# Kernel tuning notes

Hardware: AMD Instinct MI355X
Metric: run time of the kernel (lower is better)

Reference implementation:

```python
import jax, jax.numpy as jnp
import numpy as np

EPS = 1e-5

def layer_norm(x, w, b):
    mu = jnp.mean(x, axis=-1, keepdims=True)
    var = jnp.mean(jnp.square(x - mu), axis=-1, keepdims=True)
    return (x - mu) * jax.lax.rsqrt(var + EPS) * w + b

def setup_inputs() -> dict:
    key = jax.random.key(0)
    ks = jax.random.split(key, 16)
    B, N, c_z, c_h = 1, 512, 128, 128
    s_z = 1.0 / np.sqrt(c_z)
    s_h = 1.0 / np.sqrt(c_h)
    return {
        "z": jax.random.normal(ks[0], (B, N, N, c_z), jnp.float32),
        "mask": jnp.ones((B, N, N), jnp.float32),
        "norm_in_w": jnp.ones((c_z,), jnp.float32),
        "norm_in_b": jnp.zeros((c_z,), jnp.float32),
        "a_p_w": jax.random.normal(ks[1], (c_h, c_z), jnp.float32) * s_z,
        "a_p_b": jnp.zeros((c_h,), jnp.float32),
        "a_g_w": jax.random.normal(ks[2], (c_h, c_z), jnp.float32) * s_z,
        "a_g_b": jnp.ones((c_h,), jnp.float32),
        "b_p_w": jax.random.normal(ks[3], (c_h, c_z), jnp.float32) * s_z,
        "b_p_b": jnp.zeros((c_h,), jnp.float32),
        "b_g_w": jax.random.normal(ks[4], (c_h, c_z), jnp.float32) * s_z,
        "b_g_b": jnp.ones((c_h,), jnp.float32),
        "g_w": jax.random.normal(ks[5], (c_z, c_z), jnp.float32) * s_z,
        "g_b": jnp.ones((c_z,), jnp.float32),
        "z_w": jax.random.normal(ks[6], (c_z, c_h), jnp.float32) * s_h,
        "z_b": jnp.zeros((c_z,), jnp.float32),
        "norm_out_w": jnp.ones((c_h,), jnp.float32),
        "norm_out_b": jnp.zeros((c_h,), jnp.float32),
    }

OUTGOING = True

def reference(z, mask, norm_in_w, norm_in_b, a_p_w, a_p_b, a_g_w, a_g_b,
              b_p_w, b_p_b, b_g_w, b_g_b, g_w, g_b, z_w, z_b,
              norm_out_w, norm_out_b):
    # z: [B, N, N, c_z]; mask: [B, N, N]
    m = mask[..., None]  # [B, N, N, 1]
    zn = layer_norm(z, norm_in_w, norm_in_b)
    # gated projections (nn.Linear layout: W is [out, in])
    a = m * jax.nn.sigmoid(zn @ a_g_w.T + a_g_b) * (zn @ a_p_w.T + a_p_b)
    b = m * jax.nn.sigmoid(zn @ b_g_w.T + b_g_b) * (zn @ b_p_w.T + b_p_b)
    if OUTGOING:
        # x[i,j,c] = sum_k a[i,k,c] * b[j,k,c]
        x = jnp.einsum('bikc,bjkc->bijc', a, b)
    else:
        x = jnp.einsum('bkic,bkjc->bijc', a, b)
    x = layer_norm(x, norm_out_w, norm_out_b)
    x = x @ z_w.T + z_b
    g = jax.nn.sigmoid(zn @ g_w.T + g_b)
    return x * g
```

## Files before the change

### kernel.cpp

```cpp
#include <hip/hip_runtime.h>
#include <stddef.h>

#define NN 512
#define CC 128
#define NPOS (NN*NN)
#define CPITCH (NPOS + 512)

typedef unsigned short u16;
typedef unsigned int   u32;
typedef u16  u16x4  __attribute__((ext_vector_type(4)));
typedef u16  u16x8  __attribute__((ext_vector_type(8)));
typedef __bf16 bf16x8 __attribute__((ext_vector_type(8)));
typedef float f32x4  __attribute__((ext_vector_type(4)));

__device__ __forceinline__ float b2f(u16 u) {
    union { u32 i; float f; } w; w.i = ((u32)u) << 16; return w.f;
}
__device__ __forceinline__ u16 f2b(float f) {
    return __builtin_bit_cast(u16, (__bf16)f);
}
__device__ __forceinline__ float sigm(float x) { return 1.0f / (1.0f + __expf(-x)); }

__device__ __forceinline__ void gld16(const u16* g, u16* l) {
    __builtin_amdgcn_global_load_lds(
        (const __attribute__((address_space(1))) u32*)g,
        (__attribute__((address_space(3))) u32*)l, 16, 0, 0);
}

struct W6 { const float* p[6]; };

__global__ __launch_bounds__(256) void k0_pack(W6 w, u16* __restrict__ dst)
{
    const int i = blockIdx.x * 256 + threadIdx.x;
    const int mt = i >> 14, r = i & 16383;
    const int cb = r >> 11, ks = (r >> 9) & 3, lane = (r >> 3) & 63, j = r & 7;
    const int row = cb * 16 + (lane & 15);
    const int col = ks * 32 + (lane >> 4) * 8 + j;
    dst[i] = f2b(w.p[mt][row * 128 + col]);
}

__global__ __launch_bounds__(512) void k1_ln_proj(
    const float* __restrict__ z,  const float* __restrict__ mask,
    const float* __restrict__ wi, const float* __restrict__ bi,
    const u16* __restrict__ wpk,
    const float* __restrict__ agb, const float* __restrict__ apb,
    const float* __restrict__ bgb, const float* __restrict__ bpb,
    u16* __restrict__ a_cm, u16* __restrict__ b_cm,
    u16* __restrict__ zn_pm)
{
    __shared__ u16   zn[128][136];
    __shared__ float mk_lds[128];
    const int tid = threadIdx.x;
    const size_t p0 = (size_t)blockIdx.x * 128;

    if (tid < 128) mk_lds[tid] = mask[p0 + tid];

    {
        const int g  = tid >> 5;
        const int c4 = (tid & 31) * 4;
        const f32x4 wi4 = *(const f32x4*)(wi + c4);
        const f32x4 bi4 = *(const f32x4*)(bi + c4);
        f32x4 v[8];
        #pragma unroll
        for (int h = 0; h < 8; ++h)
            v[h] = *(const f32x4*)(z + (p0 + h * 16 + g) * CC + c4);
        #pragma unroll
        for (int h = 0; h < 8; ++h) {
            float s  = (v[h][0] + v[h][1]) + (v[h][2] + v[h][3]);
            float s2 = (v[h][0]*v[h][0] + v[h][1]*v[h][1])
                     + (v[h][2]*v[h][2] + v[h][3]*v[h][3]);
            #pragma unroll
            for (int ms = 1; ms <= 16; ms <<= 1) {
                s  += __shfl_xor(s,  ms);
                s2 += __shfl_xor(s2, ms);
            }
            const float mu   = s * (1.0f / CC);
            const float rstd = rsqrtf(s2 * (1.0f / CC) - mu * mu + 1e-5f);
            u16x4 o4;
            #pragma unroll
            for (int e = 0; e < 4; ++e) {
                const float nw = rstd * wi4[e];
                o4[e] = f2b(v[h][e] * nw + __builtin_fmaf(-mu, nw, bi4[e]));
            }
            const int row = h * 16 + g;
            *(u16x4*)&zn[row][c4] = o4;
            if (zn_pm)
                *(u16x4*)(zn_pm + (p0 + row) * CC + c4) = o4;
        }
    }

    const int wave = tid >> 6, lane = tid & 63;
    const int m = lane & 15, q = lane >> 4;
    const int cb = wave;
    const int o  = cb * 16 + m;

    bf16x8 wreg[4][4];
    float  bias4[4];
    {
        const float* Bv[4] = { agb, apb, bgb, bpb };
        #pragma unroll
        for (int mt = 0; mt < 4; ++mt) {
            bias4[mt] = Bv[mt][o];
            const u16* wp = wpk + ((size_t)((mt * 8 + cb) * 4)) * 512
                                + (size_t)lane * 8;
            #pragma unroll
            for (int ks = 0; ks < 4; ++ks)
                wreg[mt][ks] = *(const bf16x8*)(wp + ks * 512);
        }
    }
    __syncthreads();

    #pragma unroll 2
    for (int t = 0; t < 8; ++t) {
        bf16x8 af[4];
        #pragma unroll
        for (int ks = 0; ks < 4; ++ks)
            af[ks] = *(const bf16x8*)&zn[t * 16 + m][ks * 32 + q * 8];
        const f32x4 mk4 = *(const f32x4*)&mk_lds[t * 16 + q * 4];

        f32x4 res[4];
        #pragma unroll
        for (int mt = 0; mt < 4; ++mt) {
            const float bv = bias4[mt];
            res[mt] = f32x4{ bv, bv, bv, bv };
        }
        #pragma unroll
        for (int ks = 0; ks < 4; ++ks)
            #pragma unroll
            for (int mt = 0; mt < 4; ++mt)
                res[mt] = __builtin_amdgcn_mfma_f32_16x16x32_bf16(
                            af[ks], wreg[mt][ks], res[mt], 0, 0, 0);

        u16x4 av, bv;
        #pragma unroll
        for (int r = 0; r < 4; ++r) {
            const float mk = mk4[r];
            av[r] = f2b(mk * sigm(res[0][r]) * res[1][r]);
            bv[r] = f2b(mk * sigm(res[2][r]) * res[3][r]);
        }
        const size_t off = (size_t)o * CPITCH + p0 + t * 16 + q * 4;
        *(u16x4*)(a_cm + off) = av;
        *(u16x4*)(b_cm + off) = bv;
    }
}

__global__ __launch_bounds__(256) void k2_gemm(
    const u16* __restrict__ A, const u16* __restrict__ B, u16* __restrict__ X)
{
    __shared__ u16 As[2][128][32];
    __shared__ u16 Bs[2][128][32];
    const int tid = threadIdx.x;
    const int bx  = blockIdx.x;
    const int xcd  = bx & 7;
    const int slot = bx >> 3;
    const int c    = (slot >> 4) * 8 + xcd;
    const int tile = slot & 15;
    const int i0   = (tile >> 2) * 128;
    const int j0   = (tile & 3) * 128;
    const size_t cbase = (size_t)c * CPITCH;
    const u16* Ac = A + cbase;
    const u16* Bc = B + cbase;

    const int wave = tid >> 6, lane = tid & 63;
    const int wm = wave >> 1, wn = wave & 1;
    const int m = lane & 15, q = lane >> 4;

    f32x4 acc[4][4];
    const f32x4 zero = { 0.f, 0.f, 0.f, 0.f };
    #pragma unroll
    for (int mt = 0; mt < 4; ++mt)
        #pragma unroll
        for (int nt = 0; nt < 4; ++nt) acc[mt][nt] = zero;

    auto stage = [&](int kt, int buf) {
        #pragma unroll
        for (int ps = 0; ps < 2; ++ps) {
            const int id = ps * 256 + tid;
            const int rw = id >> 2;
            const int g  = (id & 3) ^ ((rw >> 1) & 3);
            const size_t goff = (size_t)(kt * 32 + g * 8);
            gld16(Ac + (size_t)(i0 + rw) * NN + goff, &As[buf][0][0] + id * 8);
            gld16(Bc + (size_t)(j0 + rw) * NN + goff, &Bs[buf][0][0] + id * 8);
        }
    };
    auto compute = [&](int buf) {
        bf16x8 af[4], bf[4];
        #pragma unroll
        for (int mt = 0; mt < 4; ++mt) {
            const int row = wm * 64 + mt * 16 + m;
            const int slt = q ^ ((row >> 1) & 3);
            af[mt] = *(const bf16x8*)&As[buf][row][slt * 8];
        }
        #pragma unroll
        for (int nt = 0; nt < 4; ++nt) {
            const int row = wn * 64 + nt * 16 + m;
            const int slt = q ^ ((row >> 1) & 3);
            bf[nt] = *(const bf16x8*)&Bs[buf][row][slt * 8];
        }
        #pragma unroll
        for (int mt = 0; mt < 4; ++mt)
            #pragma unroll
            for (int nt = 0; nt < 4; ++nt)
                acc[mt][nt] = __builtin_amdgcn_mfma_f32_16x16x32_bf16(
                                af[mt], bf[nt], acc[mt][nt], 0, 0, 0);
    };

    stage(0, 0);
    int cur = 0;
    for (int kt = 0; kt < 15; ++kt) {
        stage(kt + 1, cur ^ 1);
        asm volatile("s_waitcnt vmcnt(4)" ::: "memory");
        __builtin_amdgcn_s_barrier();
        __builtin_amdgcn_sched_barrier(0);
        compute(cur);
        __builtin_amdgcn_sched_barrier(0);
        __builtin_amdgcn_s_barrier();
        cur ^= 1;
    }
    asm volatile("s_waitcnt vmcnt(0)" ::: "memory");
    __builtin_amdgcn_s_barrier();
    __builtin_amdgcn_sched_barrier(0);
    compute(cur);

    #pragma unroll
    for (int mt = 0; mt < 4; ++mt) {
        #pragma unroll
        for (int r = 0; r < 4; ++r) {
            const int i = i0 + wm * 64 + mt * 16 + q * 4 + r;
            #pragma unroll
            for (int nt = 0; nt < 4; ++nt) {
                const int j = j0 + wn * 64 + nt * 16 + m;
                X[cbase + (size_t)i * NN + j] = f2b(acc[mt][nt][r]);
            }
        }
    }
}

__global__ __launch_bounds__(256) void k3_out_zn(
    float* __restrict__ out, const u16* __restrict__ x_cm,
    const u16* __restrict__ zn_pm,
    const float* __restrict__ wo, const float* __restrict__ bo,
    const u16* __restrict__ wpk,
    const float* __restrict__ gbv, const float* __restrict__ zbv)
{
    __shared__ u16 A[128][136];
    __shared__ u16 Bt[128][136];
    const int tid = threadIdx.x;
    const size_t p0 = (size_t)blockIdx.x * 128;
    const int wave = tid >> 6, lane = tid & 63;
    const int m = lane & 15, q = lane >> 4;
    const int pl = tid >> 1, ht = tid & 1;

    {
        const int c = tid >> 1, seg = tid & 1;
        #pragma unroll
        for (int e = 0; e < 8; ++e) {
            u16x8 vv = *(const u16x8*)(x_cm + (size_t)c * CPITCH + p0 + seg * 64 + e * 8);
            *(u16x8*)&Bt[c][seg * 64 + e * 8] = vv;
        }
    }
    bf16x8 afz[2][4];
    #pragma unroll
    for (int t = 0; t < 2; ++t)
        #pragma unroll
        for (int ks = 0; ks < 4; ++ks)
            afz[t][ks] = *(const bf16x8*)(zn_pm
                           + (p0 + wave * 32 + t * 16 + m) * CC + ks * 32 + q * 8);
    __syncthreads();

    {
        float v[64];
        #pragma unroll
        for (int e = 0; e < 64; ++e) v[e] = b2f(Bt[ht * 64 + e][pl]);
        float s = 0.f, s2 = 0.f;
        #pragma unroll
        for (int e = 0; e < 64; ++e) { s += v[e]; s2 += v[e] * v[e]; }
        s  += __shfl_xor(s, 1);
        s2 += __shfl_xor(s2, 1);
        const float mu   = s * (1.0f / CC);
        const float rstd = rsqrtf(s2 * (1.0f / CC) - mu * mu + 1e-5f);
        #pragma unroll
        for (int h = 0; h < 8; ++h) {
            u16x8 o8;
            #pragma unroll
            for (int e = 0; e < 8; ++e) {
                const int c = ht * 64 + h * 8 + e;
                o8[e] = f2b((v[h * 8 + e] - mu) * rstd * wo[c] + bo[c]);
            }
            *(u16x8*)&A[pl][ht * 64 + h * 8] = o8;
        }
    }
    __syncthreads();

    bf16x8 afx[2][4];
    #pragma unroll
    for (int t = 0; t < 2; ++t)
        #pragma unroll
        for (int ks = 0; ks < 4; ++ks)
            afx[t][ks] = *(const bf16x8*)&A[wave * 32 + t * 16 + m][ks * 32 + q * 8];

    for (int cb = 0; cb < 8; ++cb) {
        const int o = cb * 16 + m;
        const float gb0 = gbv[o], zb0 = zbv[o];
        f32x4 accg[2], accx[2];
        #pragma unroll
        for (int t = 0; t < 2; ++t) {
            accg[t] = f32x4{ gb0, gb0, gb0, gb0 };
            accx[t] = f32x4{ zb0, zb0, zb0, zb0 };
        }
        const u16* wpg = wpk + ((size_t)((4 * 8 + cb) * 4)) * 512 + (size_t)lane * 8;
        const u16* wpz = wpk + ((size_t)((5 * 8 + cb) * 4)) * 512 + (size_t)lane * 8;
        bf16x8 wg[4], wz[4];
        #pragma unroll
        for (int ks = 0; ks < 4; ++ks) {
            wg[ks] = *(const bf16x8*)(wpg + ks * 512);
            wz[ks] = *(const bf16x8*)(wpz + ks * 512);
        }
        #pragma unroll
        for (int ks = 0; ks < 4; ++ks)
            #pragma unroll
            for (int t = 0; t < 2; ++t) {
                accg[t] = __builtin_amdgcn_mfma_f32_16x16x32_bf16(
                            afz[t][ks], wg[ks], accg[t], 0, 0, 0);
                accx[t] = __builtin_amdgcn_mfma_f32_16x16x32_bf16(
                            afx[t][ks], wz[ks], accx[t], 0, 0, 0);
            }
        #pragma unroll
        for (int t = 0; t < 2; ++t)
            #pragma unroll
            for (int r = 0; r < 4; ++r) {
                const size_t p = p0 + wave * 32 + t * 16 + q * 4 + r;
                out[p * CC + o] = accx[t][r] * sigm(accg[t][r]);
            }
    }
}

__global__ __launch_bounds__(256) void k3_out(
    float* __restrict__ out, const u16* __restrict__ x_cm,
    const float* __restrict__ z,
    const float* __restrict__ wi, const float* __restrict__ bi,
    const float* __restrict__ wo, const float* __restrict__ bo,
    const u16* __restrict__ wpk,
    const float* __restrict__ gbv, const float* __restrict__ zbv)
{
    __shared__ u16 A[128][136];
    __shared__ u16 Bt[128][136];
    const int tid = threadIdx.x;
    const size_t p0 = (size_t)blockIdx.x * 128;
    const int wave = tid >> 6, lane = tid & 63;
    const int m = lane & 15, q = lane >> 4;
    const int pl = tid >> 1, ht = tid & 1;

    {
        const float* zr = z + (p0 + pl) * CC + ht * 64;
        float v[64];
        #pragma unroll
        for (int h = 0; h < 16; ++h) {
            f32x4 t = *(const f32x4*)(zr + h * 4);
            #pragma unroll
            for (int e = 0; e < 4; ++e) v[h * 4 + e] = t[e];
        }
        float s = 0.f, s2 = 0.f;
        #pragma unroll
        for (int e = 0; e < 64; ++e) { s += v[e]; s2 += v[e] * v[e]; }
        s  += __shfl_xor(s, 1);
        s2 += __shfl_xor(s2, 1);
        const float mu   = s * (1.0f / CC);
        const float rstd = rsqrtf(s2 * (1.0f / CC) - mu * mu + 1e-5f);
        #pragma unroll
        for (int h = 0; h < 8; ++h) {
            u16x8 o8;
            #pragma unroll
            for (int e = 0; e < 8; ++e) {
                const int c = ht * 64 + h * 8 + e;
                o8[e] = f2b((v[h * 8 + e] - mu) * rstd * wi[c] + bi[c]);
            }
            *(u16x8*)&A[pl][ht * 64 + h * 8] = o8;
        }
    }
    {
        const int c = tid >> 1, seg = tid & 1;
        #pragma unroll
        for (int e = 0; e < 8; ++e) {
            u16x8 vv = *(const u16x8*)(x_cm + (size_t)c * CPITCH + p0 + seg * 64 + e * 8);
            *(u16x8*)&Bt[c][seg * 64 + e * 8] = vv;
        }
    }
    __syncthreads();

    bf16x8 afz[2][4];
    #pragma unroll
    for (int t = 0; t < 2; ++t)
        #pragma unroll
        for (int ks = 0; ks < 4; ++ks)
            afz[t][ks] = *(const bf16x8*)&A[wave * 32 + t * 16 + m][ks * 32 + q * 8];
    __syncthreads();

    {
        float v[64];
        #pragma unroll
        for (int e = 0; e < 64; ++e) v[e] = b2f(Bt[ht * 64 + e][pl]);
        float s = 0.f, s2 = 0.f;
        #pragma unroll
        for (int e = 0; e < 64; ++e) { s += v[e]; s2 += v[e] * v[e]; }
        s  += __shfl_xor(s, 1);
        s2 += __shfl_xor(s2, 1);
        const float mu   = s * (1.0f / CC);
        const float rstd = rsqrtf(s2 * (1.0f / CC) - mu * mu + 1e-5f);
        #pragma unroll
        for (int h = 0; h < 8; ++h) {
            u16x8 o8;
            #pragma unroll
            for (int e = 0; e < 8; ++e) {
                const int c = ht * 64 + h * 8 + e;
                o8[e] = f2b((v[h * 8 + e] - mu) * rstd * wo[c] + bo[c]);
            }
            *(u16x8*)&A[pl][ht * 64 + h * 8] = o8;
        }
    }
    __syncthreads();

    bf16x8 afx[2][4];
    #pragma unroll
    for (int t = 0; t < 2; ++t)
        #pragma unroll
        for (int ks = 0; ks < 4; ++ks)
            afx[t][ks] = *(const bf16x8*)&A[wave * 32 + t * 16 + m][ks * 32 + q * 8];

    for (int cb = 0; cb < 8; ++cb) {
        const int o = cb * 16 + m;
        const float gb0 = gbv[o], zb0 = zbv[o];
        f32x4 accg[2], accx[2];
        #pragma unroll
        for (int t = 0; t < 2; ++t) {
            accg[t] = f32x4{ gb0, gb0, gb0, gb0 };
            accx[t] = f32x4{ zb0, zb0, zb0, zb0 };
        }
        const u16* wpg = wpk + ((size_t)((4 * 8 + cb) * 4)) * 512 + (size_t)lane * 8;
        const u16* wpz = wpk + ((size_t)((5 * 8 + cb) * 4)) * 512 + (size_t)lane * 8;
        bf16x8 wg[4], wz[4];
        #pragma unroll
        for (int ks = 0; ks < 4; ++ks) {
            wg[ks] = *(const bf16x8*)(wpg + ks * 512);
            wz[ks] = *(const bf16x8*)(wpz + ks * 512);
        }
        #pragma unroll
        for (int ks = 0; ks < 4; ++ks)
            #pragma unroll
            for (int t = 0; t < 2; ++t) {
                accg[t] = __builtin_amdgcn_mfma_f32_16x16x32_bf16(
                            afz[t][ks], wg[ks], accg[t], 0, 0, 0);
                accx[t] = __builtin_amdgcn_mfma_f32_16x16x32_bf16(
                            afx[t][ks], wz[ks], accx[t], 0, 0, 0);
            }
        #pragma unroll
        for (int t = 0; t < 2; ++t)
            #pragma unroll
            for (int r = 0; r < 4; ++r) {
                const size_t p = p0 + wave * 32 + t * 16 + q * 4 + r;
                out[p * CC + o] = accx[t][r] * sigm(accg[t][r]);
            }
    }
}

extern "C" void kernel_launch(void* const* d_in, const int* in_sizes, int n_in,
                              void* d_out, int out_size, void* d_ws, size_t ws_size,
                              hipStream_t stream)
{
    const float* z    = (const float*)d_in[0];
    const float* mask = (const float*)d_in[1];
    const float* wi   = (const float*)d_in[2];
    const float* bi   = (const float*)d_in[3];
    const float* apw  = (const float*)d_in[4];
    const float* apb  = (const float*)d_in[5];
    const float* agw  = (const float*)d_in[6];
    const float* agb  = (const float*)d_in[7];
    const float* bpw  = (const float*)d_in[8];
    const float* bpb  = (const float*)d_in[9];
    const float* bgw  = (const float*)d_in[10];
    const float* bgb  = (const float*)d_in[11];
    const float* gw   = (const float*)d_in[12];
    const float* gb   = (const float*)d_in[13];
    const float* zw   = (const float*)d_in[14];
    const float* zb   = (const float*)d_in[15];
    const float* wo   = (const float*)d_in[16];
    const float* bo   = (const float*)d_in[17];

    u16* a_cm = (u16*)d_ws;
    u16* b_cm = a_cm + (size_t)CC * CPITCH;
    u16* x_cm = b_cm + (size_t)CC * CPITCH;
    u16* w_pk = x_cm + (size_t)CC * CPITCH;
    u16* zn_pm = w_pk + (size_t)6 * 16384;
    float* out = (float*)d_out;

    const size_t need_zn =
        ((size_t)CC * CPITCH * 3 + 6 * 16384 + (size_t)NPOS * CC) * sizeof(u16);
    const bool use_zn = (ws_size == 0) || (ws_size >= need_zn);
    if (!use_zn) zn_pm = nullptr;

    W6 w6; w6.p[0] = agw; w6.p[1] = apw; w6.p[2] = bgw; w6.p[3] = bpw;
    w6.p[4] = gw; w6.p[5] = zw;

    k0_pack<<<6 * 16384 / 256, 256, 0, stream>>>(w6, w_pk);
    k1_ln_proj<<<NPOS / 128, 512, 0, stream>>>(z, mask, wi, bi, w_pk,
                                               agb, apb, bgb, bpb, a_cm, b_cm, zn_pm);
    k2_gemm<<<128 * 16, 256, 0, stream>>>(a_cm, b_cm, x_cm);
    if (use_zn)
        k3_out_zn<<<NPOS / 128, 256, 0, stream>>>(out, x_cm, zn_pm, wo, bo,
                                                  w_pk, gb, zb);
    else
        k3_out<<<NPOS / 128, 256, 0, stream>>>(out, x_cm, z, wi, bi, wo, bo,
                                               w_pk, gb, zb);
}
```

Before: 480.0 us.

## Rework output kernel: 8 waves per output block, swizzled LDS transpose, shuffle LayerNorm

The final output kernel now runs 512 threads, with each wave owning one 16-column output block across all 128 positions. Previously 4 waves each looped over all 8 column blocks. Projection weights stay in registers, and zn fragments are prefetched one tile ahead. The x transpose goes into a single XOR-swizzled LDS buffer that is normalized in place using 32-lane shuffle reductions, which removes the second LDS array and the strided per-thread column reads. This cuts LDS footprint and bank conflicts and adds parallelism, at the cost of scalar 2-byte LDS scatter writes during the transpose.

```diff
diff --git a/kernel.cpp b/kernel.cpp
--- a/kernel.cpp
+++ b/kernel.cpp
@@ -236,102 +236,123 @@
     }
 }
 
-__global__ __launch_bounds__(256) void k3_out_zn(
+#define XPITCH 132
+
+__global__ __launch_bounds__(512) void k3_out_v3(
     float* __restrict__ out, const u16* __restrict__ x_cm,
     const u16* __restrict__ zn_pm,
     const float* __restrict__ wo, const float* __restrict__ bo,
     const u16* __restrict__ wpk,
     const float* __restrict__ gbv, const float* __restrict__ zbv)
 {
-    __shared__ u16 A[128][136];
-    __shared__ u16 Bt[128][136];
+    __shared__ u16 XT[128 * XPITCH];
+    char* xt = (char*)XT;
     const int tid = threadIdx.x;
     const size_t p0 = (size_t)blockIdx.x * 128;
     const int wave = tid >> 6, lane = tid & 63;
     const int m = lane & 15, q = lane >> 4;
-    const int pl = tid >> 1, ht = tid & 1;
-
-    {
-        const int c = tid >> 1, seg = tid & 1;
-        #pragma unroll
-        for (int e = 0; e < 8; ++e) {
-            u16x8 vv = *(const u16x8*)(x_cm + (size_t)c * CPITCH + p0 + seg * 64 + e * 8);
-            *(u16x8*)&Bt[c][seg * 64 + e * 8] = vv;
-        }
-    }
-    bf16x8 afz[2][4];
-    #pragma unroll
-    for (int t = 0; t < 2; ++t)
-        #pragma unroll
-        for (int ks = 0; ks < 4; ++ks)
-            afz[t][ks] = *(const bf16x8*)(zn_pm
-                           + (p0 + wave * 32 + t * 16 + m) * CC + ks * 32 + q * 8);
-    __syncthreads();
-
-    {
-        float v[64];
-        #pragma unroll
-        for (int e = 0; e < 64; ++e) v[e] = b2f(Bt[ht * 64 + e][pl]);
-        float s = 0.f, s2 = 0.f;
-        #pragma unroll
-        for (int e = 0; e < 64; ++e) { s += v[e]; s2 += v[e] * v[e]; }
-        s  += __shfl_xor(s, 1);
-        s2 += __shfl_xor(s2, 1);
-        const float mu   = s * (1.0f / CC);
-        const float rstd = rsqrtf(s2 * (1.0f / CC) - mu * mu + 1e-5f);
-        #pragma unroll
-        for (int h = 0; h < 8; ++h) {
-            u16x8 o8;
-            #pragma unroll
-            for (int e = 0; e < 8; ++e) {
-                const int c = ht * 64 + h * 8 + e;
-                o8[e] = f2b((v[h * 8 + e] - mu) * rstd * wo[c] + bo[c]);
-            }
-            *(u16x8*)&A[pl][ht * 64 + h * 8] = o8;
-        }
-    }
-    __syncthreads();
-
-    bf16x8 afx[2][4];
-    #pragma unroll
-    for (int t = 0; t < 2; ++t)
-        #pragma unroll
-        for (int ks = 0; ks < 4; ++ks)
-            afx[t][ks] = *(const bf16x8*)&A[wave * 32 + t * 16 + m][ks * 32 + q * 8];
-
-    for (int cb = 0; cb < 8; ++cb) {
-        const int o = cb * 16 + m;
-        const float gb0 = gbv[o], zb0 = zbv[o];
-        f32x4 accg[2], accx[2];
-        #pragma unroll
-        for (int t = 0; t < 2; ++t) {
-            accg[t] = f32x4{ gb0, gb0, gb0, gb0 };
-            accx[t] = f32x4{ zb0, zb0, zb0, zb0 };
-        }
+
+    const int cb = wave, o = cb * 16 + m;
+    const float gb0 = gbv[o], zb0 = zbv[o];
+    bf16x8 wg[4], wz[4];
+    {
         const u16* wpg = wpk + ((size_t)((4 * 8 + cb) * 4)) * 512 + (size_t)lane * 8;
         const u16* wpz = wpk + ((size_t)((5 * 8 + cb) * 4)) * 512 + (size_t)lane * 8;
-        bf16x8 wg[4], wz[4];
         #pragma unroll
         for (int ks = 0; ks < 4; ++ks) {
             wg[ks] = *(const bf16x8*)(wpg + ks * 512);
             wz[ks] = *(const bf16x8*)(wpz + ks * 512);
         }
-        #pragma unroll
-        for (int ks = 0; ks < 4; ++ks)
-            #pragma unroll
-            for (int t = 0; t < 2; ++t) {
-                accg[t] = __builtin_amdgcn_mfma_f32_16x16x32_bf16(
-                            afz[t][ks], wg[ks], accg[t], 0, 0, 0);
-                accx[t] = __builtin_amdgcn_mfma_f32_16x16x32_bf16(
-                            afx[t][ks], wz[ks], accx[t], 0, 0, 0);
-            }
-        #pragma unroll
-        for (int t = 0; t < 2; ++t)
-            #pragma unroll
-            for (int r = 0; r < 4; ++r) {
-                const size_t p = p0 + wave * 32 + t * 16 + q * 4 + r;
-                out[p * CC + o] = accx[t][r] * sigm(accg[t][r]);
-            }
+    }
+    bf16x8 afz0[4];
+    #pragma unroll
+    for (int ks = 0; ks < 4; ++ks)
+        afz0[ks] = *(const bf16x8*)(zn_pm + (p0 + m) * CC + ks * 32 + q * 8);
+
+    {
+        const int c   = tid >> 2;
+        const int sg  = tid & 3;
+        const int key = sg << 5;
+        const int cx  = (c * 2) ^ key;
+        #pragma unroll
+        for (int l = 0; l < 4; ++l) {
+            u16x8 vv = *(const u16x8*)(x_cm + (size_t)c * CPITCH
+                                       + p0 + sg * 32 + l * 8);
+            #pragma unroll
+            for (int j = 0; j < 8; ++j) {
+                const int p = sg * 32 + l * 8 + j;
+                *(u16*)(xt + p * 264 + cx) = vv[j];
+            }
+        }
+    }
+    __syncthreads();
+
+    {
+        const int g = tid >> 5, l32 = tid & 31;
+        const int c4 = l32 * 4;
+        const f32x4 wo4 = *(const f32x4*)(wo + c4);
+        const f32x4 bo4 = *(const f32x4*)(bo + c4);
+        #pragma unroll
+        for (int h = 0; h < 8; ++h) {
+            const int r  = g * 8 + h;
+            const int ad = r * 264 + ((c4 * 2) ^ (((r >> 5) & 3) << 5));
+            const u16x4 xv = *(const u16x4*)(xt + ad);
+            const float x0 = b2f(xv[0]), x1 = b2f(xv[1]),
+                        x2 = b2f(xv[2]), x3 = b2f(xv[3]);
+            float s  = (x0 + x1) + (x2 + x3);
+            float s2 = (x0*x0 + x1*x1) + (x2*x2 + x3*x3);
+            #pragma unroll
+            for (int ms = 1; ms <= 16; ms <<= 1) {
+                s  += __shfl_xor(s,  ms);
+                s2 += __shfl_xor(s2, ms);
+            }
+            const float mu   = s * (1.0f / CC);
+            const float rstd = rsqrtf(s2 * (1.0f / CC) - mu * mu + 1e-5f);
+            u16x4 o4;
+            o4[0] = f2b((x0 - mu) * rstd * wo4[0] + bo4[0]);
+            o4[1] = f2b((x1 - mu) * rstd * wo4[1] + bo4[1]);
+            o4[2] = f2b((x2 - mu) * rstd * wo4[2] + bo4[2]);
+            o4[3] = f2b((x3 - mu) * rstd * wo4[3] + bo4[3]);
+            *(u16x4*)(xt + ad) = o4;
+        }
+    }
+    __syncthreads();
+
+    union B8 { struct { u16x4 lo, hi; } h; bf16x8 v; };
+    #pragma unroll
+    for (int t = 0; t < 8; ++t) {
+        bf16x8 afz[4];
+        #pragma unroll
+        for (int ks = 0; ks < 4; ++ks) afz[ks] = afz0[ks];
+        if (t < 7) {
+            #pragma unroll
+            for (int ks = 0; ks < 4; ++ks)
+                afz0[ks] = *(const bf16x8*)(zn_pm + (p0 + (t + 1) * 16 + m) * CC
+                                            + ks * 32 + q * 8);
+        }
+        const int key = ((t >> 1) & 3) << 5;
+        const int rowb = (t * 16 + m) * 264;
+        bf16x8 afx[4];
+        #pragma unroll
+        for (int ks = 0; ks < 4; ++ks) {
+            B8 u;
+            const int cbyte = (ks * 64 + q * 16) ^ key;
+            u.h.lo = *(const u16x4*)(xt + rowb + cbyte);
+            u.h.hi = *(const u16x4*)(xt + rowb + cbyte + 8);
+            afx[ks] = u.v;
+        }
+        f32x4 accg = { gb0, gb0, gb0, gb0 };
+        f32x4 accx = { zb0, zb0, zb0, zb0 };
+        #pragma unroll
+        for (int ks = 0; ks < 4; ++ks) {
+            accg = __builtin_amdgcn_mfma_f32_16x16x32_bf16(afz[ks], wg[ks], accg, 0, 0, 0);
+            accx = __builtin_amdgcn_mfma_f32_16x16x32_bf16(afx[ks], wz[ks], accx, 0, 0, 0);
+        }
+        #pragma unroll
+        for (int r = 0; r < 4; ++r) {
+            const size_t p = p0 + t * 16 + q * 4 + r;
+            out[p * CC + o] = accx[r] * sigm(accg[r]);
+        }
     }
 }
 
@@ -506,7 +527,7 @@
                                                agb, apb, bgb, bpb, a_cm, b_cm, zn_pm);
     k2_gemm<<<128 * 16, 256, 0, stream>>>(a_cm, b_cm, x_cm);
     if (use_zn)
-        k3_out_zn<<<NPOS / 128, 256, 0, stream>>>(out, x_cm, zn_pm, wo, bo,
+        k3_out_v3<<<NPOS / 128, 512, 0, stream>>>(out, x_cm, zn_pm, wo, bo,
                                                   w_pk, gb, zb);
     else
         k3_out<<<NPOS / 128, 256, 0, stream>>>(out, x_cm, z, wi, bi, wo, bo,
```

After: 477.0 us. About the same (-0.6%).
